# Kernel tuning notes

Hardware: AMD Instinct MI355X
Metric: run time of the kernel (lower is better)

## Reference

```python
import jax, jax.numpy as jnp
import numpy as np

B, C_OUT, DIM_I, DIM_J, DIM_K = 4, 32, 32, 32, 32


def setup_inputs() -> dict:
    key = jax.random.key(0)
    k1, k2, k3 = jax.random.split(key, 3)
    L = DIM_I * DIM_J * DIM_K
    ys = jax.random.normal(k1, (B, 12, C_OUT, L), jnp.float32)
    # Conv3d(12*c_out, c_out, kernel_size=1) -> pointwise, weight [c_out, 12*c_out]
    conv_w = jax.random.normal(k2, (C_OUT, 12 * C_OUT), jnp.float32) / np.sqrt(12 * C_OUT).astype(np.float32)
    conv_b = jax.random.normal(k3, (C_OUT,), jnp.float32) * 0.01
    gamma = jnp.ones((C_OUT,), jnp.float32)
    beta = jnp.zeros((C_OUT,), jnp.float32)
    return {"ys": ys, "conv_w": conv_w, "conv_b": conv_b,
            "gamma": gamma, "beta": beta, "i": DIM_I, "j": DIM_J, "k": DIM_K}


def _merge(x, i, j, k):
    # x: [B, 4, C, L] with L = i*j*k; 4 scan directions
    Bd, _, C, L = x.shape
    x0, x1, x2, x3 = x[:, 0], x[:, 1], x[:, 2], x[:, 3]
    # forward scans + flipped reverse scans, concat on channel dim
    x_0_2 = jnp.concatenate([x0, x2[..., ::-1]], axis=1)  # [B, 2C, L]
    x_1_3 = jnp.concatenate([x1, x3[..., ::-1]], axis=1)  # [B, 2C, L]
    a = x_0_2.reshape(Bd, 2 * C, i, j, k)
    b = x_1_3.reshape(Bd, 2 * C, i, k, j).swapaxes(-2, -1)  # transpose(-2,-1)
    return jnp.concatenate([a, b], axis=1)  # [B, 4C, i, j, k]


def reference(ys, conv_w, conv_b, gamma, beta, i, j, k):
    # ys: [B, 12, C, i*j*k]
    xs_i = _merge(ys[:, 0:4], i, j, k)                                  # [B,4C,i,j,k]
    xs_j = jnp.transpose(_merge(ys[:, 4:8], j, k, i), (0, 1, 4, 2, 3))  # b c j k i -> b c i j k
    xs_k = jnp.transpose(_merge(ys[:, 8:12], k, i, j), (0, 1, 3, 4, 2)) # b c k i j -> b c i j k
    xs = jnp.concatenate([xs_i, xs_j, xs_k], axis=1)                    # [B,12C,i,j,k]
    # 1x1x1 Conv3d == channel GEMM
    out = jnp.einsum('bcijk,oc->boijk', xs, conv_w) + conv_b[None, :, None, None, None]
    # BatchNorm3d, training mode: batch stats over (B, i, j, k), biased var, eps=1e-5
    mean = out.mean(axis=(0, 2, 3, 4))
    var = out.var(axis=(0, 2, 3, 4))
    eps = 1e-5
    inv = jax.lax.rsqrt(var + eps)
    out = (out - mean[None, :, None, None, None]) * inv[None, :, None, None, None]
    return out * gamma[None, :, None, None, None] + beta[None, :, None, None, None]
```

## Files before the change

kernel.cpp:

```cpp
#include <hip/hip_runtime.h>
#include <stdint.h>

#define COUT 32

typedef __attribute__((address_space(3))) unsigned int as3u;
typedef __attribute__((address_space(1))) unsigned int as1u;

__device__ __forceinline__ void phase_params(int ph, int& src, int& Si, int& Sj, int& Sk,
                                             int& rb, int& cb) {
  const int g = ph >> 2, q = ph & 3;
  const int neg = q & 1, v = q >> 1;
  src = (ph & ~3) | (neg << 1) | v;
  rb = neg ? 32767 : 0;
  const int sA = v ? 1 : 32, sB = v ? 32 : 1;
  if (g == 0)      { Si = 1024; Sj = sA; Sk = sB; }
  else if (g == 1) { Sj = 1024; Sk = sA; Si = sB; }
  else             { Sk = 1024; Si = sA; Sj = sB; }
  if (neg) { Si = -Si; Sj = -Sj; Sk = -Sk; }
  cb = ((g == 1) && (v == 0)) || ((g == 2) && (v == 1));
}

__device__ __forceinline__ int phase_cb(int ph) {
  const int g = ph >> 2, v = (ph >> 1) & 1;
  return ((g == 1) && (v == 0)) || ((g == 2) && (v == 1));
}

__device__ __forceinline__ void stage_phase(
    const float* __restrict__ ys, float* lbuf, int ph,
    int b, int i0, int j0, int k0, int wv, int lhi, int llo)
{
  int s, Si, Sj, Sk, rb, cb;
  phase_params(ph, s, Si, Sj, Sk, rb, cb);
  const float* ybase = ys + (((size_t)((b*12 + s)*COUT + wv*4)) << 15);
  if (!cb) {
    const int sc0 = rb + i0*Si + j0*Sj + k0*Sk + lhi*Sj + llo*Sk;
#pragma unroll
    for (int cc = 0; cc < 4; ++cc) {
#pragma unroll
      for (int pr = 0; pr < 8; ++pr) {
        const float* src = ybase + (((size_t)cc) << 15) + (sc0 + pr*Si);
        float* dst = lbuf + (wv*4 + cc)*512 + pr*64;
        __builtin_amdgcn_global_load_lds((const as1u*)src, (as3u*)dst, 4, 0, 0);
      }
    }
  } else {
    const int e   = llo ^ lhi;
    const int sc0 = rb + i0*Si + j0*Sj + k0*Sk + lhi*Sk;
#pragma unroll
    for (int cc = 0; cc < 4; ++cc) {
#pragma unroll
      for (int pr = 0; pr < 8; ++pr) {
        const int diq = e ^ pr;
        const float* src = ybase + (((size_t)cc) << 15) + (sc0 + pr*Sj + diq*Si);
        float* dst = lbuf + (wv*4 + cc)*512 + pr*64;
        __builtin_amdgcn_global_load_lds((const as1u*)src, (as3u*)dst, 4, 0, 0);
      }
    }
  }
}

__device__ __forceinline__ void stage_weights(const float* __restrict__ w, float* wbuf,
                                              int ph, int lane) {
  const float* src0 = w + ph*32 + (lane >> 3)*384 + (lane & 7)*4;
#pragma unroll
  for (int qq = 0; qq < 4; ++qq) {
    __builtin_amdgcn_global_load_lds((const as1u*)(src0 + qq*8*384),
                                     (as3u*)(wbuf + qq*256), 16, 0, 0);
  }
}

__device__ __forceinline__ void compute_phase(
    const float* wbuf, const float* lbuf, int sidx, float* acc)
{
#pragma unroll
  for (int c4 = 0; c4 < 8; ++c4) {
    const float x0 = lbuf[(c4*4+0)*512 + sidx];
    const float x1 = lbuf[(c4*4+1)*512 + sidx];
    const float x2 = lbuf[(c4*4+2)*512 + sidx];
    const float x3 = lbuf[(c4*4+3)*512 + sidx];
#pragma unroll
    for (int o = 0; o < COUT; ++o) {
      const float4 wq = *(const float4*)(wbuf + o*32 + c4*4);
      acc[o] = __builtin_fmaf(x0, wq.x, acc[o]);
      acc[o] = __builtin_fmaf(x1, wq.y, acc[o]);
      acc[o] = __builtin_fmaf(x2, wq.z, acc[o]);
      acc[o] = __builtin_fmaf(x3, wq.w, acc[o]);
    }
  }
}

__global__ __launch_bounds__(512, 2) void k_fused(
    const float* __restrict__ ys, const float* __restrict__ w,
    const float* __restrict__ cb, float* __restrict__ out)
{
  __shared__ float lds[2][COUT*512];
  __shared__ float wlds[2][COUT*32];
  const int tid  = threadIdx.x;
  const int lane = tid & 63, wv = tid >> 6;
  const int lhi  = lane >> 3, llo = lane & 7;
  const int bid  = blockIdx.x;
  const int b  = bid >> 6;
  const int i0 = ((bid >> 4) & 3) * 8;
  const int j0 = ((bid >> 2) & 3) * 8;
  const int k0 = (bid & 3) * 8;

  const int di = tid >> 6, dj = (tid >> 3) & 7, dk = tid & 7;
  const int sidxA = tid;
  const int sidxB = dj*64 + dk*8 + (di ^ dk ^ dj);

  float acc[COUT];
#pragma unroll
  for (int o = 0; o < COUT; ++o) acc[o] = 0.f;

  stage_phase(ys, &lds[0][0], 0, b, i0, j0, k0, wv, lhi, llo);
  if (wv == 0) stage_weights(w, &wlds[0][0], 0, lane);
  for (int ph = 0; ph < 12; ++ph) {
    const float* cur  = &lds[ph & 1][0];
    const float* wcur = &wlds[ph & 1][0];
    if (ph < 11) {
      stage_phase(ys, &lds[(ph + 1) & 1][0], ph + 1, b, i0, j0, k0, wv, lhi, llo);
      if (wv == 0) {
        stage_weights(w, &wlds[(ph + 1) & 1][0], ph + 1, lane);
        asm volatile("s_waitcnt vmcnt(36)" ::: "memory");
      } else {
        asm volatile("s_waitcnt vmcnt(32)" ::: "memory");
      }
    } else {
      asm volatile("s_waitcnt vmcnt(0)" ::: "memory");
    }
    __builtin_amdgcn_s_barrier();
    const int sidx = phase_cb(ph) ? sidxB : sidxA;
    compute_phase(wcur, cur, sidx, acc);
    asm volatile("" ::: "memory");
    __builtin_amdgcn_s_barrier();
  }

  const int gpos = (i0 + di)*1024 + (j0 + dj)*32 + (k0 + dk);
  float* op = out + ((((size_t)b) * COUT) << 15) + gpos;
#pragma unroll
  for (int o = 0; o < COUT; ++o)
    op[((size_t)o) << 15] = acc[o] + cb[o];
}

__global__ __launch_bounds__(256, 4) void k_stats(
    const float* __restrict__ out, float* __restrict__ stats)
{
  __shared__ float red[8];
  const int row = blockIdx.x >> 2, quad = blockIdx.x & 3;
  const int o   = row & 31;
  const int tid = threadIdx.x;
  const float* p = out + (((size_t)row) << 15) + quad * 8192;
  float s1 = 0.f, s2 = 0.f;
#pragma unroll
  for (int it = 0; it < 8; ++it) {
    const float4 v = *(const float4*)(p + it*1024 + tid*4);
    s1 += (v.x + v.y) + (v.z + v.w);
    s2 += (v.x*v.x + v.y*v.y) + (v.z*v.z + v.w*v.w);
  }
#pragma unroll
  for (int off = 32; off > 0; off >>= 1) {
    s1 += __shfl_down(s1, off, 64);
    s2 += __shfl_down(s2, off, 64);
  }
  if ((tid & 63) == 0) { red[(tid >> 6)*2] = s1; red[(tid >> 6)*2 + 1] = s2; }
  __syncthreads();
  if (tid == 0) {
    atomicAdd(&stats[o],      red[0] + red[2] + red[4] + red[6]);
    atomicAdd(&stats[32 + o], red[1] + red[3] + red[5] + red[7]);
  }
}

__global__ __launch_bounds__(256, 4) void k_norm(
    float* __restrict__ out, const float* __restrict__ stats,
    const float* __restrict__ gamma, const float* __restrict__ beta)
{
  const int row = blockIdx.x >> 2, quad = blockIdx.x & 3;
  const int o   = row & 31;
  const int tid = threadIdx.x;
  const float invN = 1.0f / 131072.0f;
  const float mean = stats[o] * invN;
  const float var  = stats[32 + o] * invN - mean*mean;
  const float inv  = rsqrtf(var + 1e-5f);
  const float sc   = gamma[o] * inv;
  const float sh   = beta[o] - mean * sc;
  float* p = out + (((size_t)row) << 15) + quad * 8192;
#pragma unroll
  for (int it = 0; it < 8; ++it) {
    float4 v = *(const float4*)(p + it*1024 + tid*4);
    v.x = __builtin_fmaf(v.x, sc, sh);
    v.y = __builtin_fmaf(v.y, sc, sh);
    v.z = __builtin_fmaf(v.z, sc, sh);
    v.w = __builtin_fmaf(v.w, sc, sh);
    *(float4*)(p + it*1024 + tid*4) = v;
  }
}

extern "C" void kernel_launch(void* const* d_in, const int* in_sizes, int n_in,
                              void* d_out, int out_size, void* d_ws, size_t ws_size,
                              hipStream_t stream)
{
  const float* ys    = (const float*)d_in[0];
  const float* w     = (const float*)d_in[1];
  const float* cb    = (const float*)d_in[2];
  const float* gamma = (const float*)d_in[3];
  const float* beta  = (const float*)d_in[4];
  float* out   = (float*)d_out;
  float* stats = (float*)d_ws;

  hipMemsetAsync(stats, 0, 64 * sizeof(float), stream);
  hipLaunchKernelGGL(k_fused, dim3(256), dim3(512), 0, stream, ys, w, cb, out);
  hipLaunchKernelGGL(k_stats, dim3(512), dim3(256), 0, stream, out, stats);
  hipLaunchKernelGGL(k_norm,  dim3(512), dim3(256), 0, stream, out, stats, gamma, beta);
}
```

Measured before the change: 424.5 us.

## Fuse batch-stat reduction into GEMM epilogue and retile threads to 8x4 outputs

Each thread now computes 8 output channels by 4 spatial positions instead of 32 channels by 1 position. Weights are read straight from global memory through a wave-uniform pointer rather than staged in LDS. The per-channel sum and sum-of-squares are reduced in the GEMM epilogue with shuffles and atomics into 8 sharded slots, which removes the separate stats kernel and its re-read of the output. This trades a kernel launch and a full output pass for more atomics and a reworked LDS read pattern (vector reads for one class of phases, strided scalar reads for the other), which may cause bank conflicts.

```diff
diff --git a/kernel.cpp b/kernel.cpp
--- a/kernel.cpp
+++ b/kernel.cpp
@@ -7,7 +7,7 @@
 typedef __attribute__((address_space(1))) unsigned int as1u;
 
 __device__ __forceinline__ void phase_params(int ph, int& src, int& Si, int& Sj, int& Sk,
-                                             int& rb, int& cb) {
+                                             int& rb, int& cbf) {
   const int g = ph >> 2, q = ph & 3;
   const int neg = q & 1, v = q >> 1;
   src = (ph & ~3) | (neg << 1) | v;
@@ -17,7 +17,7 @@
   else if (g == 1) { Sj = 1024; Sk = sA; Si = sB; }
   else             { Sk = 1024; Si = sA; Sj = sB; }
   if (neg) { Si = -Si; Sj = -Sj; Sk = -Sk; }
-  cb = ((g == 1) && (v == 0)) || ((g == 2) && (v == 1));
+  cbf = ((g == 1) && (v == 0)) || ((g == 2) && (v == 1));
 }
 
 __device__ __forceinline__ int phase_cb(int ph) {
@@ -27,12 +27,13 @@
 
 __device__ __forceinline__ void stage_phase(
     const float* __restrict__ ys, float* lbuf, int ph,
-    int b, int i0, int j0, int k0, int wv, int lhi, int llo)
-{
-  int s, Si, Sj, Sk, rb, cb;
-  phase_params(ph, s, Si, Sj, Sk, rb, cb);
+    int b, int i0, int j0, int k0, int wv, int lane)
+{
+  int s, Si, Sj, Sk, rb, cbf;
+  phase_params(ph, s, Si, Sj, Sk, rb, cbf);
+  const int lhi = lane >> 3, llo = lane & 7;
   const float* ybase = ys + (((size_t)((b*12 + s)*COUT + wv*4)) << 15);
-  if (!cb) {
+  if (!cbf) {
     const int sc0 = rb + i0*Si + j0*Sj + k0*Sk + lhi*Sj + llo*Sk;
 #pragma unroll
     for (int cc = 0; cc < 4; ++cc) {
@@ -44,14 +45,12 @@
       }
     }
   } else {
-    const int e   = llo ^ lhi;
-    const int sc0 = rb + i0*Si + j0*Sj + k0*Sk + lhi*Sk;
+    const int sc0 = rb + i0*Si + j0*Sj + k0*Sk + lhi*Sj + (llo ^ lhi)*Si;
 #pragma unroll
     for (int cc = 0; cc < 4; ++cc) {
 #pragma unroll
       for (int pr = 0; pr < 8; ++pr) {
-        const int diq = e ^ pr;
-        const float* src = ybase + (((size_t)cc) << 15) + (sc0 + pr*Sj + diq*Si);
+        const float* src = ybase + (((size_t)cc) << 15) + (sc0 + pr*Sk);
         float* dst = lbuf + (wv*4 + cc)*512 + pr*64;
         __builtin_amdgcn_global_load_lds((const as1u*)src, (as3u*)dst, 4, 0, 0);
       }
@@ -59,127 +58,131 @@
   }
 }
 
-__device__ __forceinline__ void stage_weights(const float* __restrict__ w, float* wbuf,
-                                              int ph, int lane) {
-  const float* src0 = w + ph*32 + (lane >> 3)*384 + (lane & 7)*4;
-#pragma unroll
-  for (int qq = 0; qq < 4; ++qq) {
-    __builtin_amdgcn_global_load_lds((const as1u*)(src0 + qq*8*384),
-                                     (as3u*)(wbuf + qq*256), 16, 0, 0);
-  }
-}
-
 __device__ __forceinline__ void compute_phase(
-    const float* wbuf, const float* lbuf, int sidx, float* acc)
+    const float* __restrict__ wb, const float* lbuf, int classB,
+    int storA, int storB, float acc[8][4])
 {
 #pragma unroll
   for (int c4 = 0; c4 < 8; ++c4) {
-    const float x0 = lbuf[(c4*4+0)*512 + sidx];
-    const float x1 = lbuf[(c4*4+1)*512 + sidx];
-    const float x2 = lbuf[(c4*4+2)*512 + sidx];
-    const float x3 = lbuf[(c4*4+3)*512 + sidx];
-#pragma unroll
-    for (int o = 0; o < COUT; ++o) {
-      const float4 wq = *(const float4*)(wbuf + o*32 + c4*4);
-      acc[o] = __builtin_fmaf(x0, wq.x, acc[o]);
-      acc[o] = __builtin_fmaf(x1, wq.y, acc[o]);
-      acc[o] = __builtin_fmaf(x2, wq.z, acc[o]);
-      acc[o] = __builtin_fmaf(x3, wq.w, acc[o]);
+    float4 ws[8];
+#pragma unroll
+    for (int oo = 0; oo < 8; ++oo)
+      ws[oo] = *(const float4*)(wb + oo*384 + c4*4);
+    float4 xv[4];
+    if (!classB) {
+#pragma unroll
+      for (int cc = 0; cc < 4; ++cc)
+        xv[cc] = *(const float4*)(lbuf + (c4*4 + cc)*512 + storA);
+    } else {
+#pragma unroll
+      for (int cc = 0; cc < 4; ++cc) {
+        const float* bp = lbuf + (c4*4 + cc)*512 + storB;
+        xv[cc].x = bp[0]; xv[cc].y = bp[64]; xv[cc].z = bp[128]; xv[cc].w = bp[192];
+      }
+    }
+#pragma unroll
+    for (int oo = 0; oo < 8; ++oo) {
+#pragma unroll
+      for (int cc = 0; cc < 4; ++cc) {
+        const float wv_ = ((const float*)&ws[oo])[cc];
+        acc[oo][0] = __builtin_fmaf(xv[cc].x, wv_, acc[oo][0]);
+        acc[oo][1] = __builtin_fmaf(xv[cc].y, wv_, acc[oo][1]);
+        acc[oo][2] = __builtin_fmaf(xv[cc].z, wv_, acc[oo][2]);
+        acc[oo][3] = __builtin_fmaf(xv[cc].w, wv_, acc[oo][3]);
+      }
     }
   }
 }
 
 __global__ __launch_bounds__(512, 2) void k_fused(
     const float* __restrict__ ys, const float* __restrict__ w,
-    const float* __restrict__ cb, float* __restrict__ out)
+    const float* __restrict__ cb, float* __restrict__ out,
+    float* __restrict__ stats)
 {
   __shared__ float lds[2][COUT*512];
-  __shared__ float wlds[2][COUT*32];
   const int tid  = threadIdx.x;
   const int lane = tid & 63, wv = tid >> 6;
-  const int lhi  = lane >> 3, llo = lane & 7;
   const int bid  = blockIdx.x;
   const int b  = bid >> 6;
   const int i0 = ((bid >> 4) & 3) * 8;
   const int j0 = ((bid >> 2) & 3) * 8;
   const int k0 = (bid & 3) * 8;
 
-  const int di = tid >> 6, dj = (tid >> 3) & 7, dk = tid & 7;
-  const int sidxA = tid;
-  const int sidxB = dj*64 + dk*8 + (di ^ dk ^ dj);
-
-  float acc[COUT];
-#pragma unroll
-  for (int o = 0; o < COUT; ++o) acc[o] = 0.f;
-
-  stage_phase(ys, &lds[0][0], 0, b, i0, j0, k0, wv, lhi, llo);
-  if (wv == 0) stage_weights(w, &wlds[0][0], 0, lane);
+  const int og = __builtin_amdgcn_readfirstlane(tid >> 7);
+  const int pg = tid & 127;
+  const int di = pg >> 4, dj = (pg >> 1) & 7, u = pg & 1;
+
+  const int storA = di*64 + dj*8 + 4*u;
+  const int storB = 256*u + 8*dj + (di ^ dj);
+
+  float acc[8][4];
+#pragma unroll
+  for (int oo = 0; oo < 8; ++oo)
+#pragma unroll
+    for (int p = 0; p < 4; ++p) acc[oo][p] = 0.f;
+
+  stage_phase(ys, &lds[0][0], 0, b, i0, j0, k0, wv, lane);
   for (int ph = 0; ph < 12; ++ph) {
-    const float* cur  = &lds[ph & 1][0];
-    const float* wcur = &wlds[ph & 1][0];
+    const float* cur = &lds[ph & 1][0];
     if (ph < 11) {
-      stage_phase(ys, &lds[(ph + 1) & 1][0], ph + 1, b, i0, j0, k0, wv, lhi, llo);
-      if (wv == 0) {
-        stage_weights(w, &wlds[(ph + 1) & 1][0], ph + 1, lane);
-        asm volatile("s_waitcnt vmcnt(36)" ::: "memory");
-      } else {
-        asm volatile("s_waitcnt vmcnt(32)" ::: "memory");
-      }
+      stage_phase(ys, &lds[(ph + 1) & 1][0], ph + 1, b, i0, j0, k0, wv, lane);
+      asm volatile("s_waitcnt vmcnt(32)" ::: "memory");
     } else {
       asm volatile("s_waitcnt vmcnt(0)" ::: "memory");
     }
     __builtin_amdgcn_s_barrier();
-    const int sidx = phase_cb(ph) ? sidxB : sidxA;
-    compute_phase(wcur, cur, sidx, acc);
+    compute_phase(w + ph*32 + og*8*384, cur, phase_cb(ph), storA, storB, acc);
     asm volatile("" ::: "memory");
     __builtin_amdgcn_s_barrier();
   }
 
-  const int gpos = (i0 + di)*1024 + (j0 + dj)*32 + (k0 + dk);
-  float* op = out + ((((size_t)b) * COUT) << 15) + gpos;
-#pragma unroll
-  for (int o = 0; o < COUT; ++o)
-    op[((size_t)o) << 15] = acc[o] + cb[o];
-}
-
-__global__ __launch_bounds__(256, 4) void k_stats(
-    const float* __restrict__ out, float* __restrict__ stats)
-{
-  __shared__ float red[8];
+  const int o0 = og*8;
+  const int gpos0 = (i0 + di)*1024 + (j0 + dj)*32 + (k0 + 4*u);
+  float s1[8], s2[8];
+#pragma unroll
+  for (int oo = 0; oo < 8; ++oo) {
+    const float bias = cb[o0 + oo];
+    float4 v;
+    v.x = acc[oo][0] + bias; v.y = acc[oo][1] + bias;
+    v.z = acc[oo][2] + bias; v.w = acc[oo][3] + bias;
+    *(float4*)(out + (((size_t)(b*COUT + o0 + oo)) << 15) + gpos0) = v;
+    s1[oo] = (v.x + v.y) + (v.z + v.w);
+    s2[oo] = (v.x*v.x + v.y*v.y) + (v.z*v.z + v.w*v.w);
+  }
+#pragma unroll
+  for (int off = 32; off > 0; off >>= 1) {
+#pragma unroll
+    for (int oo = 0; oo < 8; ++oo) {
+      s1[oo] += __shfl_down(s1[oo], off, 64);
+      s2[oo] += __shfl_down(s2[oo], off, 64);
+    }
+  }
+  if (lane == 0) {
+    float* sh = stats + (bid & 7)*64;
+#pragma unroll
+    for (int oo = 0; oo < 8; ++oo) {
+      atomicAdd(&sh[o0 + oo],      s1[oo]);
+      atomicAdd(&sh[32 + o0 + oo], s2[oo]);
+    }
+  }
+}
+
+__global__ __launch_bounds__(256, 4) void k_norm(
+    float* __restrict__ out, const float* __restrict__ stats,
+    const float* __restrict__ gamma, const float* __restrict__ beta)
+{
   const int row = blockIdx.x >> 2, quad = blockIdx.x & 3;
   const int o   = row & 31;
   const int tid = threadIdx.x;
-  const float* p = out + (((size_t)row) << 15) + quad * 8192;
-  float s1 = 0.f, s2 = 0.f;
-#pragma unroll
-  for (int it = 0; it < 8; ++it) {
-    const float4 v = *(const float4*)(p + it*1024 + tid*4);
-    s1 += (v.x + v.y) + (v.z + v.w);
-    s2 += (v.x*v.x + v.y*v.y) + (v.z*v.z + v.w*v.w);
-  }
-#pragma unroll
-  for (int off = 32; off > 0; off >>= 1) {
-    s1 += __shfl_down(s1, off, 64);
-    s2 += __shfl_down(s2, off, 64);
-  }
-  if ((tid & 63) == 0) { red[(tid >> 6)*2] = s1; red[(tid >> 6)*2 + 1] = s2; }
-  __syncthreads();
-  if (tid == 0) {
-    atomicAdd(&stats[o],      red[0] + red[2] + red[4] + red[6]);
-    atomicAdd(&stats[32 + o], red[1] + red[3] + red[5] + red[7]);
-  }
-}
-
-__global__ __launch_bounds__(256, 4) void k_norm(
-    float* __restrict__ out, const float* __restrict__ stats,
-    const float* __restrict__ gamma, const float* __restrict__ beta)
-{
-  const int row = blockIdx.x >> 2, quad = blockIdx.x & 3;
-  const int o   = row & 31;
-  const int tid = threadIdx.x;
+  float sum = 0.f, ssq = 0.f;
+#pragma unroll
+  for (int s = 0; s < 8; ++s) {
+    sum += stats[s*64 + o];
+    ssq += stats[s*64 + 32 + o];
+  }
   const float invN = 1.0f / 131072.0f;
-  const float mean = stats[o] * invN;
-  const float var  = stats[32 + o] * invN - mean*mean;
+  const float mean = sum * invN;
+  const float var  = ssq * invN - mean*mean;
   const float inv  = rsqrtf(var + 1e-5f);
   const float sc   = gamma[o] * inv;
   const float sh   = beta[o] - mean * sc;
@@ -207,8 +210,7 @@
   float* out   = (float*)d_out;
   float* stats = (float*)d_ws;
 
-  hipMemsetAsync(stats, 0, 64 * sizeof(float), stream);
-  hipLaunchKernelGGL(k_fused, dim3(256), dim3(512), 0, stream, ys, w, cb, out);
-  hipLaunchKernelGGL(k_stats, dim3(512), dim3(256), 0, stream, out, stats);
+  hipMemsetAsync(stats, 0, 8*64*sizeof(float), stream);
+  hipLaunchKernelGGL(k_fused, dim3(256), dim3(512), 0, stream, ys, w, cb, out, stats);
   hipLaunchKernelGGL(k_norm,  dim3(512), dim3(256), 0, stream, out, stats, gamma, beta);
 }
```

Result: no change. 428.3 us (+0.9%).
